# Kernel optimization log

Hardware: AMD Instinct MI355X
Metric: run time of the kernel (lower is better)

## Reference

```python
import jax, jax.numpy as jnp
import numpy as np

B, T = 1024, 1024
D_IN, UNITS, WIDTH, DEPTH, D_OUT = 6, 64, 128, 3, 6
START = UNITS + D_IN  # concat([x_normed, h]) width
EPS = 1e-8


def _xavier(key, fin, fout):
    lim = float(np.sqrt(6.0 / (fin + fout)))
    return jax.random.uniform(key, (fin, fout), minval=-lim, maxval=lim, dtype=jnp.float32)


def setup_inputs() -> dict:
    key = jax.random.key(0)
    ks = jax.random.split(key, 12)
    d = {
        "x": jax.random.normal(ks[0], (B, T, D_IN), dtype=jnp.float32),
        "init_F": jax.random.normal(ks[1], (B, 2 + UNITS), dtype=jnp.float32) * 0.1,
    }
    dims = [START] + [WIDTH] * DEPTH
    for i in range(DEPTH):
        d[f"qb1_w{i}"] = _xavier(ks[2 + 2 * i], dims[i], dims[i + 1])
        d[f"qb1_b{i}"] = jnp.zeros((dims[i + 1],), dtype=jnp.float32)
        d[f"qb2_w{i}"] = _xavier(ks[3 + 2 * i], dims[i], dims[i + 1])
        d[f"qb2_b{i}"] = jnp.zeros((dims[i + 1],), dtype=jnp.float32)
    d["wa"] = _xavier(ks[8], WIDTH, UNITS)
    d["ba"] = jnp.zeros((UNITS,), dtype=jnp.float32)
    d["wb"] = _xavier(ks[9], WIDTH, UNITS)
    d["bb"] = jnp.zeros((UNITS,), dtype=jnp.float32)
    # fc_out bias is frozen at zero in the original -> weight only
    d["wout"] = _xavier(ks[10], UNITS, D_OUT)
    return d


def reference(x, init_F,
              qb1_w0, qb1_b0, qb2_w0, qb2_b0,
              qb1_w1, qb1_b1, qb2_w1, qb2_b1,
              qb1_w2, qb1_b2, qb2_w2, qb2_b2,
              wa, ba, wb, bb, wout):
    layers = ((qb1_w0, qb1_b0, qb2_w0, qb2_b0),
              (qb1_w1, qb1_b1, qb2_w1, qb2_b1),
              (qb1_w2, qb1_b2, qb2_w2, qb2_b2))
    h0 = init_F[:, 2:2 + UNITS]  # [B, UNITS]

    def step(h, xt):  # xt: [B, D_IN], h: [B, UNITS]
        norm = jnp.sqrt(jnp.sum(xt * xt, axis=1, keepdims=True))  # [B,1]
        xn = xt / (norm + EPS)
        c = jnp.concatenate([xn, h], axis=1)  # [B, START]
        for i, (w1, b1, w2, b2) in enumerate(layers):
            x1 = c @ w1 + b1
            x2 = c @ w2 + b2
            if i < DEPTH - 1:
                x1 = jnp.tanh(x1)
                x2 = jnp.tanh(x2)
            c = x1 * x2
        g = jnp.tanh(c)
        alpha = jnp.exp(g @ wa + ba)          # [B, UNITS]
        beta = jnp.tanh(g @ wb + bb)          # [B, UNITS]
        h_new = jnp.exp(-alpha * norm) * (h - beta) + beta
        return h_new, (h_new @ wout, alpha)

    _, (outs, alphas) = jax.lax.scan(step, h0, jnp.swapaxes(x, 0, 1))
    # outs: [T,B,D_OUT], alphas: [T,B,UNITS] -> batch-major
    return jnp.swapaxes(outs, 0, 1), jnp.swapaxes(alphas, 0, 1)
```

## Files before the change

### kernel.cpp

```cpp
#include <hip/hip_runtime.h>
#include <stdint.h>
#include <stddef.h>

#define NB 1024
#define TB 1024
#define D_IN 6
#define UNITS 64
#define WIDTH 128
#define DOUT 6
#define EPSF 1e-8f
#define SPB 16
#define LDK0 108
#define LDK 140

typedef _Float16 v8h __attribute__((ext_vector_type(8)));
typedef float v4f __attribute__((ext_vector_type(4)));
typedef float v2f __attribute__((ext_vector_type(2)));

#define MFMAH(A,Bf,C) __builtin_amdgcn_mfma_f32_16x16x32_f16((A),(Bf),(C),0,0,0)

#define BARRIER_LDS() asm volatile("s_waitcnt lgkmcnt(0)\n\ts_barrier" ::: "memory")

#define C2L2E  2.8853900817779268f
#define L2E    1.4426950408889634f
#define NEGL2E (-1.4426950408889634f)

__device__ __forceinline__ float rcp_fast(float x){ return __builtin_amdgcn_rcpf(x); }

__device__ __forceinline__ float tanh_from_arg(float a2){
  float u = __builtin_amdgcn_exp2f(a2);
  return fmaf(-2.0f, rcp_fast(u + 1.0f), 1.0f);
}

__device__ __forceinline__ void make_frag1(const float* vals, v8h& hv){
  #pragma unroll
  for (int j = 0; j < 8; j++) hv[j] = (_Float16)vals[j];
}
__device__ __forceinline__ void make_frag2(const float* vals, v8h& hv, v8h& lv){
  #pragma unroll
  for (int j = 0; j < 8; j++){
    _Float16 h = (_Float16)vals[j];
    hv[j] = h;
    lv[j] = (_Float16)(vals[j] - (float)h);
  }
}

__global__ __launch_bounds__(512, 2) void lmsc_kernel(
    const float* __restrict__ x, const float* __restrict__ initF,
    const float* __restrict__ w10, const float* __restrict__ b10,
    const float* __restrict__ w20, const float* __restrict__ b20,
    const float* __restrict__ w11, const float* __restrict__ b11,
    const float* __restrict__ w21, const float* __restrict__ b21,
    const float* __restrict__ w12, const float* __restrict__ b12,
    const float* __restrict__ w22, const float* __restrict__ b22,
    const float* __restrict__ wa, const float* __restrict__ ba,
    const float* __restrict__ wb, const float* __restrict__ bb,
    const float* __restrict__ wo,
    float* __restrict__ outs, float* __restrict__ alph)
{
  __shared__ __attribute__((aligned(16))) _Float16 c0[2][SPB*LDK0];
  __shared__ __attribute__((aligned(16))) _Float16 cP[SPB*LDK];
  __shared__ __attribute__((aligned(16))) _Float16 cQ[SPB*LDK];
  __shared__ __attribute__((aligned(16))) _Float16 cG[SPB*LDK];
  __shared__ __attribute__((aligned(16))) float nrm[2][SPB];

  const int tid = threadIdx.x;
  const int wv = tid >> 6;
  const int ln = tid & 63;
  const int mn = ln & 15;
  const int qd = ln >> 4;
  const int q8 = qd * 8;
  const int n  = wv * 16 + mn;
  const int sgbase = (int)blockIdx.x * SPB;

  float tmp[8];


  v8h B0[3][2];
  #pragma unroll
  for (int kf = 0; kf < 3; kf++)
    #pragma unroll
    for (int br = 0; br < 2; br++){
      const float* W = br ? w20 : w10;
      #pragma unroll
      for (int j = 0; j < 8; j++){
        int k = kf*32 + q8 + j;
        int r = (k < 6) ? k : ((k >= 8 && k < 72) ? (k - 2) : -1);
        tmp[j] = (r >= 0) ? W[r*WIDTH + n] * C2L2E : 0.0f;
      }
      make_frag1(tmp, B0[kf][br]);
    }

  v8h B1[4][2], B2[4][2];
  #pragma unroll
  for (int kf = 0; kf < 4; kf++)
    #pragma unroll
    for (int br = 0; br < 2; br++){
      const float* W = br ? w21 : w11;
      #pragma unroll
      for (int j = 0; j < 8; j++)
        tmp[j] = W[(kf*32 + q8 + j)*WIDTH + n] * C2L2E;
      make_frag1(tmp, B1[kf][br]);
      const float* V = br ? w22 : w12;
      const float sc = br ? 1.0f : C2L2E;
      #pragma unroll
      for (int j = 0; j < 8; j++)
        tmp[j] = V[(kf*32 + q8 + j)*WIDTH + n] * sc;
      make_frag1(tmp, B2[kf][br]);
    }

  const int u = (wv & 3) * 16 + mn;
  v8h Bah[4], Bal[4], Bbh[4];
  #pragma unroll
  for (int kf = 0; kf < 4; kf++){
    #pragma unroll
    for (int j = 0; j < 8; j++)
      tmp[j] = wa[(kf*32 + q8 + j)*UNITS + u] * L2E;
    make_frag2(tmp, Bah[kf], Bal[kf]);
    #pragma unroll
    for (int j = 0; j < 8; j++)
      tmp[j] = wb[(kf*32 + q8 + j)*UNITS + u] * C2L2E;
    make_frag1(tmp, Bbh[kf]);
  }

  v8h Woh0, Woh1;
  #pragma unroll
  for (int j = 0; j < 8; j++)
    tmp[j] = (mn < DOUT) ? wo[(q8 + j)*DOUT + mn] : 0.0f;
  make_frag1(tmp, Woh0);
  #pragma unroll
  for (int j = 0; j < 8; j++)
    tmp[j] = (mn < DOUT) ? wo[(32 + q8 + j)*DOUT + mn] : 0.0f;
  make_frag1(tmp, Woh1);

  const float e0a = b10[n] * C2L2E, e0b = b20[n] * C2L2E;
  const float e1a = b11[n] * C2L2E, e1b = b21[n] * C2L2E;
  const float e2a = b12[n] * C2L2E, e2b = b22[n];
  const v4f E0A = {e0a, e0a, e0a, e0a}, E0B = {e0b, e0b, e0b, e0b};
  const v4f E1A = {e1a, e1a, e1a, e1a}, E1B = {e1b, e1b, e1b, e1b};
  const v4f E2A = {e2a, e2a, e2a, e2a}, E2B = {e2b, e2b, e2b, e2b};
  const float bsa = ba[u] * L2E;
  const float bsb = bb[u] * C2L2E;
  const v4f BSA4 = {bsa, bsa, bsa, bsa};
  const v4f BSB4 = {bsb, bsb, bsb, bsb};
  const v4f Z4   = {0.f, 0.f, 0.f, 0.f};

  float* alp  = alph + ((size_t)(sgbase + qd*4) * TB) * UNITS + u;
  float* outp = outs + ((size_t)(sgbase + qd*4) * TB) * DOUT + mn;

  for (int i = tid; i < 2*SPB*LDK0; i += 512) c0[0][i] = (_Float16)0.0f;
  __syncthreads();

  float hreg[4];
  if (wv < 4){
    #pragma unroll
    for (int r = 0; r < 4; r++){
      int s = qd*4 + r;
      float v = initF[(size_t)(sgbase + s)*(2 + UNITS) + 2 + u];
      hreg[r] = v;
      c0[0][s*LDK0 + 8 + u] = (_Float16)v;
    }
  }
  float xv0=0, xv1=0, xv2=0, xv3=0, xv4=0, xv5=0;
  if (wv == 4 && ln < 16){
    const v2f* xp2 = (const v2f*)(x + (size_t)(sgbase + ln)*TB*D_IN);
    v2f A = xp2[0], Bv = xp2[1], C = xp2[2];
    float nv = sqrtf(A[0]*A[0] + A[1]*A[1] + Bv[0]*Bv[0] + Bv[1]*Bv[1] + C[0]*C[0] + C[1]*C[1]);
    nrm[0][ln] = nv * NEGL2E;
    float inv = 1.0f / (nv + EPSF);
    c0[0][ln*LDK0 + 0] = (_Float16)(A[0]*inv);
    c0[0][ln*LDK0 + 1] = (_Float16)(A[1]*inv);
    c0[0][ln*LDK0 + 2] = (_Float16)(Bv[0]*inv);
    c0[0][ln*LDK0 + 3] = (_Float16)(Bv[1]*inv);
    c0[0][ln*LDK0 + 4] = (_Float16)(C[0]*inv);
    c0[0][ln*LDK0 + 5] = (_Float16)(C[1]*inv);
    v2f D = xp2[3], E = xp2[4], F = xp2[5];
    xv0 = D[0]; xv1 = D[1]; xv2 = E[0]; xv3 = E[1]; xv4 = F[0]; xv5 = F[1];
  }
  __syncthreads();

  auto wout_phase = [&](const _Float16* cb, int tt){
    v8h ah0 = *(const v8h*)(cb + mn*LDK0 + 8 + q8);
    v8h ah1 = *(const v8h*)(cb + mn*LDK0 + 40 + q8);
    v4f acc = MFMAH(ah0, Woh0, Z4);
    acc = MFMAH(ah1, Woh1, acc);
    if (mn < DOUT){
      #pragma unroll
      for (int r = 0; r < 4; r++)
        outp[(size_t)r*TB*DOUT + (size_t)tt*DOUT] = acc[r];
    }
  };

  if (wv < 4) __builtin_amdgcn_s_setprio(1);

  for (int t = 0; t < TB; t++){
    const int p = t & 1;
    const _Float16* c0r = c0[p];
    _Float16* c0w = c0[p ^ 1];

    {
      v8h ah[3];
      #pragma unroll
      for (int kf = 0; kf < 3; kf++)
        ah[kf] = *(const v8h*)(c0r + mn*LDK0 + kf*32 + q8);
      v4f acc0 = MFMAH(ah[0], B0[0][0], E0A);
      v4f acc1 = MFMAH(ah[0], B0[0][1], E0B);
      acc0 = MFMAH(ah[1], B0[1][0], acc0);
      acc1 = MFMAH(ah[1], B0[1][1], acc1);
      acc0 = MFMAH(ah[2], B0[2][0], acc0);
      acc1 = MFMAH(ah[2], B0[2][1], acc1);
      #pragma unroll
      for (int r = 0; r < 4; r++){
        float u0 = __builtin_amdgcn_exp2f(acc0[r]);
        float u1 = __builtin_amdgcn_exp2f(acc1[r]);
        float pr = u0 * u1;
        float sm = u0 + u1;
        float pp = pr + 1.0f;
        float res = (pp - sm) * rcp_fast(pp + sm);
        cP[(qd*4 + r)*LDK + n] = (_Float16)res;
      }
    }
    BARRIER_LDS();

    {
      v8h ah[4];
      #pragma unroll
      for (int kf = 0; kf < 4; kf++)
        ah[kf] = *(const v8h*)(cP + mn*LDK + kf*32 + q8);
      v4f acc0 = MFMAH(ah[0], B1[0][0], E1A);
      v4f acc1 = MFMAH(ah[0], B1[0][1], E1B);
      acc0 = MFMAH(ah[1], B1[1][0], acc0);
      acc1 = MFMAH(ah[1], B1[1][1], acc1);
      acc0 = MFMAH(ah[2], B1[2][0], acc0);
      acc1 = MFMAH(ah[2], B1[2][1], acc1);
      acc0 = MFMAH(ah[3], B1[3][0], acc0);
      acc1 = MFMAH(ah[3], B1[3][1], acc1);
      #pragma unroll
      for (int r = 0; r < 4; r++){
        float u0 = __builtin_amdgcn_exp2f(acc0[r]);
        float u1 = __builtin_amdgcn_exp2f(acc1[r]);
        float pr = u0 * u1;
        float sm = u0 + u1;
        float pp = pr + 1.0f;
        float res = (pp - sm) * rcp_fast(pp + sm);
        cQ[(qd*4 + r)*LDK + n] = (_Float16)res;
      }
    }
    BARRIER_LDS();

    {
      v8h ah[4];
      #pragma unroll
      for (int kf = 0; kf < 4; kf++)
        ah[kf] = *(const v8h*)(cQ + mn*LDK + kf*32 + q8);
      v4f acc0 = MFMAH(ah[0], B2[0][0], E2A);
      v4f acc1 = MFMAH(ah[0], B2[0][1], E2B);
      acc0 = MFMAH(ah[1], B2[1][0], acc0);
      acc1 = MFMAH(ah[1], B2[1][1], acc1);
      acc0 = MFMAH(ah[2], B2[2][0], acc0);
      acc1 = MFMAH(ah[2], B2[2][1], acc1);
      acc0 = MFMAH(ah[3], B2[3][0], acc0);
      acc1 = MFMAH(ah[3], B2[3][1], acc1);
      #pragma unroll
      for (int r = 0; r < 4; r++)
        cG[(qd*4 + r)*LDK + n] = (_Float16)tanh_from_arg(acc0[r] * acc1[r]);
    }
    BARRIER_LDS();

    if (wv < 4){
      v8h gh[4];
      #pragma unroll
      for (int kf = 0; kf < 4; kf++)
        gh[kf] = *(const v8h*)(cG + mn*LDK + kf*32 + q8);
      v4f pA0 = MFMAH(gh[0], Bah[0], BSA4);
      v4f pA1 = MFMAH(gh[2], Bah[2], Z4);
      v4f pB  = MFMAH(gh[0], Bbh[0], BSB4);
      pA0 = MFMAH(gh[0], Bal[0], pA0);
      pA1 = MFMAH(gh[2], Bal[2], pA1);
      pB  = MFMAH(gh[1], Bbh[1], pB);
      pA0 = MFMAH(gh[1], Bah[1], pA0);
      pA1 = MFMAH(gh[3], Bah[3], pA1);
      pB  = MFMAH(gh[2], Bbh[2], pB);
      pA0 = MFMAH(gh[1], Bal[1], pA0);
      pA1 = MFMAH(gh[3], Bal[3], pA1);
      pB  = MFMAH(gh[3], Bbh[3], pB);
      #pragma unroll
      for (int r = 0; r < 4; r++){
        int s = qd*4 + r;
        float m = nrm[p][s];
        float alpha = __builtin_amdgcn_exp2f(pA0[r] + pA1[r]);
        float beta  = tanh_from_arg(pB[r]);
        float dec   = __builtin_amdgcn_exp2f(alpha * m);
        float h = fmaf(dec, hreg[r] - beta, beta);
        hreg[r] = h;
        c0w[s*LDK0 + 8 + u] = (_Float16)h;
        alp[(size_t)r*TB*UNITS] = alpha;
      }
      alp += UNITS;
    } else if (wv == 7){
      if (t > 0) wout_phase(c0r, t - 1);
    } else if (wv == 4 && ln < 16){
      float nv2 = sqrtf(xv0*xv0 + xv1*xv1 + xv2*xv2 + xv3*xv3 + xv4*xv4 + xv5*xv5);
      nrm[p ^ 1][ln] = nv2 * NEGL2E;
      float inv = 1.0f / (nv2 + EPSF);
      c0w[ln*LDK0 + 0] = (_Float16)(xv0*inv);
      c0w[ln*LDK0 + 1] = (_Float16)(xv1*inv);
      c0w[ln*LDK0 + 2] = (_Float16)(xv2*inv);
      c0w[ln*LDK0 + 3] = (_Float16)(xv3*inv);
      c0w[ln*LDK0 + 4] = (_Float16)(xv4*inv);
      c0w[ln*LDK0 + 5] = (_Float16)(xv5*inv);
      int tn = t + 2; if (tn > TB - 1) tn = TB - 1;
      const v2f* xp2 = (const v2f*)(x + ((size_t)(sgbase + ln)*TB + (size_t)tn)*D_IN);
      v2f D = xp2[0], E = xp2[1], F = xp2[2];
      xv0 = D[0]; xv1 = D[1]; xv2 = E[0]; xv3 = E[1]; xv4 = F[0]; xv5 = F[1];
    }
    BARRIER_LDS();
  }

  if (wv == 7) wout_phase(c0[TB & 1], TB - 1);
}

extern "C" void kernel_launch(void* const* d_in, const int* in_sizes, int n_in,
                              void* d_out, int out_size, void* d_ws, size_t ws_size,
                              hipStream_t stream) {
  const float* x    = (const float*)d_in[0];
  const float* iF   = (const float*)d_in[1];
  const float* w10  = (const float*)d_in[2];
  const float* b10  = (const float*)d_in[3];
  const float* w20  = (const float*)d_in[4];
  const float* b20  = (const float*)d_in[5];
  const float* w11  = (const float*)d_in[6];
  const float* b11  = (const float*)d_in[7];
  const float* w21  = (const float*)d_in[8];
  const float* b21  = (const float*)d_in[9];
  const float* w12  = (const float*)d_in[10];
  const float* b12  = (const float*)d_in[11];
  const float* w22  = (const float*)d_in[12];
  const float* b22  = (const float*)d_in[13];
  const float* wa   = (const float*)d_in[14];
  const float* ba   = (const float*)d_in[15];
  const float* wb   = (const float*)d_in[16];
  const float* bb   = (const float*)d_in[17];
  const float* wo   = (const float*)d_in[18];

  float* outs = (float*)d_out;
  float* alph = outs + (size_t)NB*TB*DOUT;

  lmsc_kernel<<<NB/SPB, 512, 0, stream>>>(x, iF,
      w10, b10, w20, b20, w11, b11, w21, b21, w12, b12, w22, b22,
      wa, ba, wb, bb, wo, outs, alph);
}
```

Measured before the change: 2.319 ms.

## Interleave two independent sequence tiles per block in a staggered phase pipeline

Each block now processes 32 sequences as two 16-sequence tiles whose recurrent chains are offset by two phases. Within each barrier interval one tile's layer work runs alongside the other tile's next layer or update, so the block does four barrier intervals per timestep for twice the sequences. The aim is to hide MFMA and transcendental latency of the serial chain and to halve the grid, keeping the block count per barrier roughly constant. It also drops the wave priority hint and doubles per-phase work and LDS buffers, which adds register pressure and lengthens each interval.

```diff
diff --git a/kernel.cpp b/kernel.cpp
--- a/kernel.cpp
+++ b/kernel.cpp
@@ -9,7 +9,8 @@
 #define WIDTH 128
 #define DOUT 6
 #define EPSF 1e-8f
-#define SPB 16
+#define SPB 32
+#define SPT 16
 #define LDK0 108
 #define LDK 140
 
@@ -43,6 +44,128 @@
     hv[j] = h;
     lv[j] = (_Float16)(vals[j] - (float)h);
   }
+}
+
+#define PH_A(c0r, cPw) { \
+  v8h ah0 = *(const v8h*)((c0r) + mn*LDK0 + 0*32 + q8); \
+  v8h ah1 = *(const v8h*)((c0r) + mn*LDK0 + 1*32 + q8); \
+  v8h ah2 = *(const v8h*)((c0r) + mn*LDK0 + 2*32 + q8); \
+  v4f acc0 = MFMAH(ah0, B0[0][0], E0A); \
+  v4f acc1 = MFMAH(ah0, B0[0][1], E0B); \
+  acc0 = MFMAH(ah1, B0[1][0], acc0); \
+  acc1 = MFMAH(ah1, B0[1][1], acc1); \
+  acc0 = MFMAH(ah2, B0[2][0], acc0); \
+  acc1 = MFMAH(ah2, B0[2][1], acc1); \
+  _Pragma("unroll") \
+  for (int r = 0; r < 4; r++){ \
+    float u0 = __builtin_amdgcn_exp2f(acc0[r]); \
+    float u1 = __builtin_amdgcn_exp2f(acc1[r]); \
+    float pp = fmaf(u0, u1, 1.0f); \
+    float sm = u0 + u1; \
+    (cPw)[(qd*4 + r)*LDK + n] = (_Float16)((pp - sm) * rcp_fast(pp + sm)); \
+  } \
+}
+
+#define PH_B(cPr, cQw) { \
+  v8h bh0 = *(const v8h*)((cPr) + mn*LDK + 0*32 + q8); \
+  v8h bh1 = *(const v8h*)((cPr) + mn*LDK + 1*32 + q8); \
+  v8h bh2 = *(const v8h*)((cPr) + mn*LDK + 2*32 + q8); \
+  v8h bh3 = *(const v8h*)((cPr) + mn*LDK + 3*32 + q8); \
+  v4f acc0 = MFMAH(bh0, B1[0][0], E1A); \
+  v4f acc1 = MFMAH(bh0, B1[0][1], E1B); \
+  acc0 = MFMAH(bh1, B1[1][0], acc0); \
+  acc1 = MFMAH(bh1, B1[1][1], acc1); \
+  acc0 = MFMAH(bh2, B1[2][0], acc0); \
+  acc1 = MFMAH(bh2, B1[2][1], acc1); \
+  acc0 = MFMAH(bh3, B1[3][0], acc0); \
+  acc1 = MFMAH(bh3, B1[3][1], acc1); \
+  _Pragma("unroll") \
+  for (int r = 0; r < 4; r++){ \
+    float u0 = __builtin_amdgcn_exp2f(acc0[r]); \
+    float u1 = __builtin_amdgcn_exp2f(acc1[r]); \
+    float pp = fmaf(u0, u1, 1.0f); \
+    float sm = u0 + u1; \
+    (cQw)[(qd*4 + r)*LDK + n] = (_Float16)((pp - sm) * rcp_fast(pp + sm)); \
+  } \
+}
+
+#define PH_C(cQr, cGw) { \
+  v8h ch0 = *(const v8h*)((cQr) + mn*LDK + 0*32 + q8); \
+  v8h ch1 = *(const v8h*)((cQr) + mn*LDK + 1*32 + q8); \
+  v8h ch2 = *(const v8h*)((cQr) + mn*LDK + 2*32 + q8); \
+  v8h ch3 = *(const v8h*)((cQr) + mn*LDK + 3*32 + q8); \
+  v4f acc0 = MFMAH(ch0, B2[0][0], E2A); \
+  v4f acc1 = MFMAH(ch0, B2[0][1], E2B); \
+  acc0 = MFMAH(ch1, B2[1][0], acc0); \
+  acc1 = MFMAH(ch1, B2[1][1], acc1); \
+  acc0 = MFMAH(ch2, B2[2][0], acc0); \
+  acc1 = MFMAH(ch2, B2[2][1], acc1); \
+  acc0 = MFMAH(ch3, B2[3][0], acc0); \
+  acc1 = MFMAH(ch3, B2[3][1], acc1); \
+  _Pragma("unroll") \
+  for (int r = 0; r < 4; r++) \
+    (cGw)[(qd*4 + r)*LDK + n] = (_Float16)tanh_from_arg(acc0[r] * acc1[r]); \
+}
+
+#define PH_D(cGr, c0w, nrp, hrg, alp_) { \
+  v8h gh0 = *(const v8h*)((cGr) + mn*LDK + 0*32 + q8); \
+  v8h gh1 = *(const v8h*)((cGr) + mn*LDK + 1*32 + q8); \
+  v8h gh2 = *(const v8h*)((cGr) + mn*LDK + 2*32 + q8); \
+  v8h gh3 = *(const v8h*)((cGr) + mn*LDK + 3*32 + q8); \
+  v4f pA0 = MFMAH(gh0, Bah[0], BSA4); \
+  v4f pA1 = MFMAH(gh2, Bah[2], Z4); \
+  v4f pB  = MFMAH(gh0, Bbh[0], BSB4); \
+  pA0 = MFMAH(gh0, Bal[0], pA0); \
+  pA1 = MFMAH(gh2, Bal[2], pA1); \
+  pB  = MFMAH(gh1, Bbh[1], pB); \
+  pA0 = MFMAH(gh1, Bah[1], pA0); \
+  pA1 = MFMAH(gh3, Bah[3], pA1); \
+  pB  = MFMAH(gh2, Bbh[2], pB); \
+  pA0 = MFMAH(gh1, Bal[1], pA0); \
+  pA1 = MFMAH(gh3, Bal[3], pA1); \
+  pB  = MFMAH(gh3, Bbh[3], pB); \
+  _Pragma("unroll") \
+  for (int r = 0; r < 4; r++){ \
+    int s = qd*4 + r; \
+    float m = (nrp)[s]; \
+    float alpha = __builtin_amdgcn_exp2f(pA0[r] + pA1[r]); \
+    float beta  = tanh_from_arg(pB[r]); \
+    float dec   = __builtin_amdgcn_exp2f(alpha * m); \
+    float h = fmaf(dec, (hrg)[r] - beta, beta); \
+    (hrg)[r] = h; \
+    (c0w)[s*LDK0 + 8 + u] = (_Float16)h; \
+    (alp_)[(size_t)r*TB*UNITS] = alpha; \
+  } \
+  (alp_) += UNITS; \
+}
+
+#define WOUT(cb, tt, outp_) { \
+  v8h wh0 = *(const v8h*)((cb) + mn*LDK0 + 8 + q8); \
+  v8h wh1 = *(const v8h*)((cb) + mn*LDK0 + 40 + q8); \
+  v4f acc = MFMAH(wh0, Woh0, Z4); \
+  acc = MFMAH(wh1, Woh1, acc); \
+  if (mn < DOUT){ \
+    _Pragma("unroll") \
+    for (int r = 0; r < 4; r++) \
+      (outp_)[(size_t)r*TB*DOUT + (size_t)(tt)*DOUT] = acc[r]; \
+  } \
+}
+
+#define XNORM(c0w, nrw, HI) { \
+  int s = ln & 15; \
+  float nv2 = sqrtf(xv0*xv0 + xv1*xv1 + xv2*xv2 + xv3*xv3 + xv4*xv4 + xv5*xv5); \
+  (nrw)[s] = nv2 * NEGL2E; \
+  float inv = 1.0f / (nv2 + EPSF); \
+  (c0w)[s*LDK0 + 0] = (_Float16)(xv0*inv); \
+  (c0w)[s*LDK0 + 1] = (_Float16)(xv1*inv); \
+  (c0w)[s*LDK0 + 2] = (_Float16)(xv2*inv); \
+  (c0w)[s*LDK0 + 3] = (_Float16)(xv3*inv); \
+  (c0w)[s*LDK0 + 4] = (_Float16)(xv4*inv); \
+  (c0w)[s*LDK0 + 5] = (_Float16)(xv5*inv); \
+  int tn = t + 2; if (tn > TB - 1) tn = TB - 1; \
+  const v2f* xp2 = (const v2f*)(x + ((size_t)(sgbase + (HI) + s)*TB + (size_t)tn)*D_IN); \
+  v2f Dv = xp2[0], Ev = xp2[1], Fv = xp2[2]; \
+  xv0 = Dv[0]; xv1 = Dv[1]; xv2 = Ev[0]; xv3 = Ev[1]; xv4 = Fv[0]; xv5 = Fv[1]; \
 }
 
 __global__ __launch_bounds__(512, 2) void lmsc_kernel(
@@ -58,11 +181,11 @@
     const float* __restrict__ wo,
     float* __restrict__ outs, float* __restrict__ alph)
 {
-  __shared__ __attribute__((aligned(16))) _Float16 c0[2][SPB*LDK0];
-  __shared__ __attribute__((aligned(16))) _Float16 cP[SPB*LDK];
-  __shared__ __attribute__((aligned(16))) _Float16 cQ[SPB*LDK];
-  __shared__ __attribute__((aligned(16))) _Float16 cG[SPB*LDK];
-  __shared__ __attribute__((aligned(16))) float nrm[2][SPB];
+  __shared__ __attribute__((aligned(16))) _Float16 c0s[2][2][SPT*LDK0];
+  __shared__ __attribute__((aligned(16))) _Float16 cPs[2][SPT*LDK];
+  __shared__ __attribute__((aligned(16))) _Float16 cQs[2][SPT*LDK];
+  __shared__ __attribute__((aligned(16))) _Float16 cGs[2][SPT*LDK];
+  __shared__ __attribute__((aligned(16))) float nrms[2][2][SPT];
 
   const int tid = threadIdx.x;
   const int wv = tid >> 6;
@@ -74,7 +197,6 @@
   const int sgbase = (int)blockIdx.x * SPB;
 
   float tmp[8];
-
 
   v8h B0[3][2];
   #pragma unroll
@@ -145,179 +267,96 @@
   const v4f BSB4 = {bsb, bsb, bsb, bsb};
   const v4f Z4   = {0.f, 0.f, 0.f, 0.f};
 
-  float* alp  = alph + ((size_t)(sgbase + qd*4) * TB) * UNITS + u;
-  float* outp = outs + ((size_t)(sgbase + qd*4) * TB) * DOUT + mn;
-
-  for (int i = tid; i < 2*SPB*LDK0; i += 512) c0[0][i] = (_Float16)0.0f;
+  float* alpE  = alph + ((size_t)(sgbase + qd*4) * TB) * UNITS + u;
+  float* alpO  = alph + ((size_t)(sgbase + SPT + qd*4) * TB) * UNITS + u;
+  float* outpE = outs + ((size_t)(sgbase + qd*4) * TB) * DOUT + mn;
+  float* outpO = outs + ((size_t)(sgbase + SPT + qd*4) * TB) * DOUT + mn;
+
+  for (int i = tid; i < 2*2*SPT*LDK0; i += 512) (&c0s[0][0][0])[i] = (_Float16)0.0f;
   __syncthreads();
 
-  float hreg[4];
+  float hregE[4], hregO[4];
   if (wv < 4){
     #pragma unroll
     for (int r = 0; r < 4; r++){
       int s = qd*4 + r;
-      float v = initF[(size_t)(sgbase + s)*(2 + UNITS) + 2 + u];
-      hreg[r] = v;
-      c0[0][s*LDK0 + 8 + u] = (_Float16)v;
+      float vE = initF[(size_t)(sgbase + s)*(2 + UNITS) + 2 + u];
+      float vO = initF[(size_t)(sgbase + SPT + s)*(2 + UNITS) + 2 + u];
+      hregE[r] = vE;
+      hregO[r] = vO;
+      c0s[0][0][s*LDK0 + 8 + u] = (_Float16)vE;
+      c0s[1][0][s*LDK0 + 8 + u] = (_Float16)vO;
     }
   }
   float xv0=0, xv1=0, xv2=0, xv3=0, xv4=0, xv5=0;
-  if (wv == 4 && ln < 16){
-    const v2f* xp2 = (const v2f*)(x + (size_t)(sgbase + ln)*TB*D_IN);
+  if (wv == 4 && ln < 32){
+    const int tl = ln >> 4, s = ln & 15;
+    const v2f* xp2 = (const v2f*)(x + (size_t)(sgbase + tl*SPT + s)*TB*D_IN);
     v2f A = xp2[0], Bv = xp2[1], C = xp2[2];
     float nv = sqrtf(A[0]*A[0] + A[1]*A[1] + Bv[0]*Bv[0] + Bv[1]*Bv[1] + C[0]*C[0] + C[1]*C[1]);
-    nrm[0][ln] = nv * NEGL2E;
+    nrms[tl][0][s] = nv * NEGL2E;
     float inv = 1.0f / (nv + EPSF);
-    c0[0][ln*LDK0 + 0] = (_Float16)(A[0]*inv);
-    c0[0][ln*LDK0 + 1] = (_Float16)(A[1]*inv);
-    c0[0][ln*LDK0 + 2] = (_Float16)(Bv[0]*inv);
-    c0[0][ln*LDK0 + 3] = (_Float16)(Bv[1]*inv);
-    c0[0][ln*LDK0 + 4] = (_Float16)(C[0]*inv);
-    c0[0][ln*LDK0 + 5] = (_Float16)(C[1]*inv);
+    _Float16* cw = &c0s[tl][0][0];
+    cw[s*LDK0 + 0] = (_Float16)(A[0]*inv);
+    cw[s*LDK0 + 1] = (_Float16)(A[1]*inv);
+    cw[s*LDK0 + 2] = (_Float16)(Bv[0]*inv);
+    cw[s*LDK0 + 3] = (_Float16)(Bv[1]*inv);
+    cw[s*LDK0 + 4] = (_Float16)(C[0]*inv);
+    cw[s*LDK0 + 5] = (_Float16)(C[1]*inv);
     v2f D = xp2[3], E = xp2[4], F = xp2[5];
     xv0 = D[0]; xv1 = D[1]; xv2 = E[0]; xv3 = E[1]; xv4 = F[0]; xv5 = F[1];
   }
   __syncthreads();
 
-  auto wout_phase = [&](const _Float16* cb, int tt){
-    v8h ah0 = *(const v8h*)(cb + mn*LDK0 + 8 + q8);
-    v8h ah1 = *(const v8h*)(cb + mn*LDK0 + 40 + q8);
-    v4f acc = MFMAH(ah0, Woh0, Z4);
-    acc = MFMAH(ah1, Woh1, acc);
-    if (mn < DOUT){
-      #pragma unroll
-      for (int r = 0; r < 4; r++)
-        outp[(size_t)r*TB*DOUT + (size_t)tt*DOUT] = acc[r];
-    }
-  };
-
-  if (wv < 4) __builtin_amdgcn_s_setprio(1);
+  PH_A(c0s[1][0], cPs[1]);
+  BARRIER_LDS();
+  PH_B(cPs[1], cQs[1]);
+  BARRIER_LDS();
 
   for (int t = 0; t < TB; t++){
     const int p = t & 1;
-    const _Float16* c0r = c0[p];
-    _Float16* c0w = c0[p ^ 1];
-
-    {
-      v8h ah[3];
-      #pragma unroll
-      for (int kf = 0; kf < 3; kf++)
-        ah[kf] = *(const v8h*)(c0r + mn*LDK0 + kf*32 + q8);
-      v4f acc0 = MFMAH(ah[0], B0[0][0], E0A);
-      v4f acc1 = MFMAH(ah[0], B0[0][1], E0B);
-      acc0 = MFMAH(ah[1], B0[1][0], acc0);
-      acc1 = MFMAH(ah[1], B0[1][1], acc1);
-      acc0 = MFMAH(ah[2], B0[2][0], acc0);
-      acc1 = MFMAH(ah[2], B0[2][1], acc1);
-      #pragma unroll
-      for (int r = 0; r < 4; r++){
-        float u0 = __builtin_amdgcn_exp2f(acc0[r]);
-        float u1 = __builtin_amdgcn_exp2f(acc1[r]);
-        float pr = u0 * u1;
-        float sm = u0 + u1;
-        float pp = pr + 1.0f;
-        float res = (pp - sm) * rcp_fast(pp + sm);
-        cP[(qd*4 + r)*LDK + n] = (_Float16)res;
-      }
-    }
+    const _Float16* c0rE = c0s[0][p];
+    _Float16* c0wE = c0s[0][p ^ 1];
+    const _Float16* c0rO = c0s[1][p];
+    _Float16* c0wO = c0s[1][p ^ 1];
+
+    PH_A(c0rE, cPs[0]);
+    PH_C(cQs[1], cGs[1]);
     BARRIER_LDS();
 
-    {
-      v8h ah[4];
-      #pragma unroll
-      for (int kf = 0; kf < 4; kf++)
-        ah[kf] = *(const v8h*)(cP + mn*LDK + kf*32 + q8);
-      v4f acc0 = MFMAH(ah[0], B1[0][0], E1A);
-      v4f acc1 = MFMAH(ah[0], B1[0][1], E1B);
-      acc0 = MFMAH(ah[1], B1[1][0], acc0);
-      acc1 = MFMAH(ah[1], B1[1][1], acc1);
-      acc0 = MFMAH(ah[2], B1[2][0], acc0);
-      acc1 = MFMAH(ah[2], B1[2][1], acc1);
-      acc0 = MFMAH(ah[3], B1[3][0], acc0);
-      acc1 = MFMAH(ah[3], B1[3][1], acc1);
-      #pragma unroll
-      for (int r = 0; r < 4; r++){
-        float u0 = __builtin_amdgcn_exp2f(acc0[r]);
-        float u1 = __builtin_amdgcn_exp2f(acc1[r]);
-        float pr = u0 * u1;
-        float sm = u0 + u1;
-        float pp = pr + 1.0f;
-        float res = (pp - sm) * rcp_fast(pp + sm);
-        cQ[(qd*4 + r)*LDK + n] = (_Float16)res;
-      }
+    PH_B(cPs[0], cQs[0]);
+    if (wv < 4){
+      PH_D(cGs[1], c0wO, nrms[1][p], hregO, alpO);
+    } else if (wv == 7){
+      if (t > 0) WOUT(c0rO, t - 1, outpO);
+    } else if (wv == 4 && (ln >> 4) == 1){
+      XNORM(c0wO, nrms[1][p ^ 1], SPT);
     }
     BARRIER_LDS();
 
-    {
-      v8h ah[4];
-      #pragma unroll
-      for (int kf = 0; kf < 4; kf++)
-        ah[kf] = *(const v8h*)(cQ + mn*LDK + kf*32 + q8);
-      v4f acc0 = MFMAH(ah[0], B2[0][0], E2A);
-      v4f acc1 = MFMAH(ah[0], B2[0][1], E2B);
-      acc0 = MFMAH(ah[1], B2[1][0], acc0);
-      acc1 = MFMAH(ah[1], B2[1][1], acc1);
-      acc0 = MFMAH(ah[2], B2[2][0], acc0);
-      acc1 = MFMAH(ah[2], B2[2][1], acc1);
-      acc0 = MFMAH(ah[3], B2[3][0], acc0);
-      acc1 = MFMAH(ah[3], B2[3][1], acc1);
-      #pragma unroll
-      for (int r = 0; r < 4; r++)
-        cG[(qd*4 + r)*LDK + n] = (_Float16)tanh_from_arg(acc0[r] * acc1[r]);
+    PH_C(cQs[0], cGs[0]);
+    if (t < TB - 1){
+      PH_A(c0wO, cPs[1]);
     }
     BARRIER_LDS();
 
+    if (t < TB - 1){
+      PH_B(cPs[1], cQs[1]);
+    }
     if (wv < 4){
-      v8h gh[4];
-      #pragma unroll
-      for (int kf = 0; kf < 4; kf++)
-        gh[kf] = *(const v8h*)(cG + mn*LDK + kf*32 + q8);
-      v4f pA0 = MFMAH(gh[0], Bah[0], BSA4);
-      v4f pA1 = MFMAH(gh[2], Bah[2], Z4);
-      v4f pB  = MFMAH(gh[0], Bbh[0], BSB4);
-      pA0 = MFMAH(gh[0], Bal[0], pA0);
-      pA1 = MFMAH(gh[2], Bal[2], pA1);
-      pB  = MFMAH(gh[1], Bbh[1], pB);
-      pA0 = MFMAH(gh[1], Bah[1], pA0);
-      pA1 = MFMAH(gh[3], Bah[3], pA1);
-      pB  = MFMAH(gh[2], Bbh[2], pB);
-      pA0 = MFMAH(gh[1], Bal[1], pA0);
-      pA1 = MFMAH(gh[3], Bal[3], pA1);
-      pB  = MFMAH(gh[3], Bbh[3], pB);
-      #pragma unroll
-      for (int r = 0; r < 4; r++){
-        int s = qd*4 + r;
-        float m = nrm[p][s];
-        float alpha = __builtin_amdgcn_exp2f(pA0[r] + pA1[r]);
-        float beta  = tanh_from_arg(pB[r]);
-        float dec   = __builtin_amdgcn_exp2f(alpha * m);
-        float h = fmaf(dec, hreg[r] - beta, beta);
-        hreg[r] = h;
-        c0w[s*LDK0 + 8 + u] = (_Float16)h;
-        alp[(size_t)r*TB*UNITS] = alpha;
-      }
-      alp += UNITS;
+      PH_D(cGs[0], c0wE, nrms[0][p], hregE, alpE);
     } else if (wv == 7){
-      if (t > 0) wout_phase(c0r, t - 1);
-    } else if (wv == 4 && ln < 16){
-      float nv2 = sqrtf(xv0*xv0 + xv1*xv1 + xv2*xv2 + xv3*xv3 + xv4*xv4 + xv5*xv5);
-      nrm[p ^ 1][ln] = nv2 * NEGL2E;
-      float inv = 1.0f / (nv2 + EPSF);
-      c0w[ln*LDK0 + 0] = (_Float16)(xv0*inv);
-      c0w[ln*LDK0 + 1] = (_Float16)(xv1*inv);
-      c0w[ln*LDK0 + 2] = (_Float16)(xv2*inv);
-      c0w[ln*LDK0 + 3] = (_Float16)(xv3*inv);
-      c0w[ln*LDK0 + 4] = (_Float16)(xv4*inv);
-      c0w[ln*LDK0 + 5] = (_Float16)(xv5*inv);
-      int tn = t + 2; if (tn > TB - 1) tn = TB - 1;
-      const v2f* xp2 = (const v2f*)(x + ((size_t)(sgbase + ln)*TB + (size_t)tn)*D_IN);
-      v2f D = xp2[0], E = xp2[1], F = xp2[2];
-      xv0 = D[0]; xv1 = D[1]; xv2 = E[0]; xv3 = E[1]; xv4 = F[0]; xv5 = F[1];
+      if (t > 0) WOUT(c0rE, t - 1, outpE);
+    } else if (wv == 4 && (ln >> 4) == 0){
+      XNORM(c0wE, nrms[0][p ^ 1], 0);
     }
     BARRIER_LDS();
   }
 
-  if (wv == 7) wout_phase(c0[TB & 1], TB - 1);
+  if (wv == 7){
+    WOUT(c0s[0][0], TB - 1, outpE);
+    WOUT(c0s[1][0], TB - 1, outpO);
+  }
 }
 
 extern "C" void kernel_launch(void* const* d_in, const int* in_sizes, int n_in,
```

After: 4.103 ms. 1.77x slower.
